# Kernel tuning notes

Measured on AMD Instinct MI355X. Metric: run time of the kernel, lower is better.

The kernel has to match this reference:

```python
import jax, jax.numpy as jnp
import numpy as np

INPUT_DIM = 1024
CODEBOOK_DIM = 128
CODEBOOK_SIZE = 8192
B, N = 8, 4096


def setup_inputs() -> dict:
    key = jax.random.key(0)
    k1, k2, k3 = jax.random.split(key, 3)
    x = jax.random.normal(k1, (B, N, INPUT_DIM), dtype=jnp.float32)
    # xavier_normal_: std = sqrt(2 / (fan_in + fan_out))
    xavier_std = float(np.sqrt(2.0 / (INPUT_DIM + CODEBOOK_DIM)))
    random_projection = jax.random.normal(k2, (INPUT_DIM, CODEBOOK_DIM), dtype=jnp.float32) * xavier_std
    codebook = jax.random.normal(k3, (CODEBOOK_SIZE, CODEBOOK_DIM), dtype=jnp.float32)
    return {"x": x, "random_projection": random_projection, "codebook": codebook}


def reference(x, random_projection, codebook):
    # random projection: [B, N, D] @ [D, E] -> [B, N, E]
    proj = jnp.einsum("bnd,de->bne", x, random_projection)
    b, n, e = proj.shape
    flat = proj.reshape(b * n, e)  # [BN, E]
    eps = 1e-12  # matches torch F.normalize default eps
    nx = flat / jnp.maximum(jnp.linalg.norm(flat, axis=1, keepdims=True), eps)
    ncb = codebook / jnp.maximum(jnp.linalg.norm(codebook, axis=1, keepdims=True), eps)
    # squared euclidean distances [K, BN]; argmin of d^2 == argmin of cdist
    d2 = (
        jnp.sum(ncb * ncb, axis=1)[:, None]
        + jnp.sum(nx * nx, axis=1)[None, :]
        - 2.0 * (ncb @ nx.T)
    )
    nearest = jnp.argmin(d2, axis=0)  # [BN]
    return nearest.reshape(b, n).astype(jnp.int32)
```

## Files before the change

kernel.cpp:

```cpp
#include <hip/hip_runtime.h>
#include <math.h>
#include <float.h>
#include <limits.h>

#define BN      32768
#define D_IN    1024
#define E_DIM   128
#define CB_N    8192

typedef _Float16 f16x8 __attribute__((ext_vector_type(8)));
typedef _Float16 f16x4 __attribute__((ext_vector_type(4)));
typedef float    f32x4 __attribute__((ext_vector_type(4)));


__global__ __launch_bounds__(256) void pack_cb_kernel(
    const float* __restrict__ cb, _Float16* __restrict__ ph,
    _Float16* __restrict__ pl) {
    __shared__ float L[16][129];
    const int t = threadIdx.x;
    const int g = blockIdx.x;

    const int c = t >> 4, p = t & 15;
    const float4 v0 = *(const float4*)&cb[(size_t)(g * 16 + c) * E_DIM + p * 8];
    const float4 v1 = *(const float4*)&cb[(size_t)(g * 16 + c) * E_DIM + p * 8 + 4];
    float ss = v0.x * v0.x + v0.y * v0.y + v0.z * v0.z + v0.w * v0.w
             + v1.x * v1.x + v1.y * v1.y + v1.z * v1.z + v1.w * v1.w;
#pragma unroll
    for (int m = 1; m < 16; m <<= 1) ss += __shfl_xor(ss, m);
    const float inv = 256.0f / fmaxf(sqrtf(ss), 1e-12f);

    L[c][p * 8 + 0] = v0.x * inv; L[c][p * 8 + 1] = v0.y * inv;
    L[c][p * 8 + 2] = v0.z * inv; L[c][p * 8 + 3] = v0.w * inv;
    L[c][p * 8 + 4] = v1.x * inv; L[c][p * 8 + 5] = v1.y * inv;
    L[c][p * 8 + 6] = v1.z * inv; L[c][p * 8 + 7] = v1.w * inv;
    __syncthreads();

    const int kb = t >> 6, lane = t & 63;
    const int quad = (lane >> 4), col = lane & 15;
    f16x8 h, l;
#pragma unroll
    for (int j = 0; j < 8; ++j) {
        const float v = L[col][kb * 32 + quad * 8 + j];
        const _Float16 hv = (_Float16)v;
        h[j] = hv;
        l[j] = (_Float16)(v - (float)hv);
    }
    const size_t off = ((size_t)(g * 4 + kb) * 64 + lane) * 8;
    *(f16x8*)&ph[off] = h;
    *(f16x8*)&pl[off] = l;
}

__global__ __launch_bounds__(64) void pack_rp_kernel(
    const float* __restrict__ rp, _Float16* __restrict__ rph,
    _Float16* __restrict__ rpl) {
    const int b = blockIdx.x;
    const int kb = b >> 3, nt = b & 7;
    const int lane = threadIdx.x;
    const int quad = lane >> 4, col = lane & 15;
    f16x8 h, l;
#pragma unroll
    for (int j = 0; j < 8; ++j) {
        const float v = rp[(size_t)(kb * 32 + quad * 8 + j) * E_DIM + nt * 16 + col] * 64.0f;
        const _Float16 hv = (_Float16)v;
        h[j] = hv;
        l[j] = (_Float16)(v - (float)hv);
    }
    const size_t off = ((size_t)b * 64 + lane) * 8;
    *(f16x8*)&rph[off] = h;
    *(f16x8*)&rpl[off] = l;
}

#define PAD_ROW 40

__global__ __launch_bounds__(256) void proj_kernel(
    const float* __restrict__ x,
    const _Float16* __restrict__ rph, const _Float16* __restrict__ rpl,
    _Float16* __restrict__ qh, _Float16* __restrict__ ql) {
    __shared__ _Float16 Ah[64 * PAD_ROW];
    __shared__ _Float16 Al[64 * PAD_ROW];

    const int tid  = threadIdx.x;
    const int lane = tid & 63;
    const int w    = tid >> 6;
    const int quad = lane >> 4, col = lane & 15;
    const int rbase = blockIdx.x * 64;

    const int srow = tid >> 3;
    const int skc  = (tid & 7) * 4;

    f32x4 acc[4][2];
#pragma unroll
    for (int mt = 0; mt < 4; ++mt)
#pragma unroll
        for (int h = 0; h < 2; ++h) acc[mt][h] = (f32x4){0.f, 0.f, 0.f, 0.f};

    float4 pre[2];
#pragma unroll
    for (int i = 0; i < 2; ++i)
        pre[i] = *(const float4*)&x[(size_t)(rbase + srow + 32 * i) * D_IN + skc];

    for (int kb = 0; kb < 32; ++kb) {
#pragma unroll
        for (int i = 0; i < 2; ++i) {
            const float vv[4] = {pre[i].x, pre[i].y, pre[i].z, pre[i].w};
            f16x4 h4, l4;
#pragma unroll
            for (int j = 0; j < 4; ++j) {
                const float v = vv[j] * 512.0f;
                const _Float16 hv = (_Float16)v;
                h4[j] = hv;
                l4[j] = (_Float16)(v - (float)hv);
            }
            const int base = (srow + 32 * i) * PAD_ROW + skc;
            *(f16x4*)&Ah[base] = h4;
            *(f16x4*)&Al[base] = l4;
        }
        __syncthreads();

        if (kb + 1 < 32) {
#pragma unroll
            for (int i = 0; i < 2; ++i)
                pre[i] = *(const float4*)&x[(size_t)(rbase + srow + 32 * i) * D_IN + (kb + 1) * 32 + skc];
        }

        f16x8 bh[2], bl[2];
#pragma unroll
        for (int h = 0; h < 2; ++h) {
            const int nt = w * 2 + h;
            const size_t off = ((size_t)(kb * 8 + nt) * 64 + lane) * 8;
            bh[h] = *(const f16x8*)&rph[off];
            bl[h] = *(const f16x8*)&rpl[off];
        }

        f16x8 ah[4], al[4];
#pragma unroll
        for (int mt = 0; mt < 4; ++mt) {
            const int base = (mt * 16 + col) * PAD_ROW + quad * 8;
            ah[mt] = *(const f16x8*)&Ah[base];
            al[mt] = *(const f16x8*)&Al[base];
        }

#pragma unroll
        for (int mt = 0; mt < 4; ++mt)
#pragma unroll
            for (int h = 0; h < 2; ++h)
                acc[mt][h] = __builtin_amdgcn_mfma_f32_16x16x32_f16(ah[mt], bh[h], acc[mt][h], 0, 0, 0);
#pragma unroll
        for (int mt = 0; mt < 4; ++mt)
#pragma unroll
            for (int h = 0; h < 2; ++h)
                acc[mt][h] = __builtin_amdgcn_mfma_f32_16x16x32_f16(ah[mt], bl[h], acc[mt][h], 0, 0, 0);
#pragma unroll
        for (int mt = 0; mt < 4; ++mt)
#pragma unroll
            for (int h = 0; h < 2; ++h)
                acc[mt][h] = __builtin_amdgcn_mfma_f32_16x16x32_f16(al[mt], bh[h], acc[mt][h], 0, 0, 0);

        __syncthreads();
    }

#pragma unroll
    for (int mt = 0; mt < 4; ++mt) {
#pragma unroll
        for (int h = 0; h < 2; ++h) {
#pragma unroll
            for (int r = 0; r < 4; ++r) {
                const float v = acc[mt][h][r] * (1.0f / 2048.0f);
                const _Float16 hv = (_Float16)v;
                const _Float16 lv = (_Float16)(v - (float)hv);
                const size_t o = (size_t)(rbase + mt * 16 + quad * 4 + r) * E_DIM
                               + w * 32 + h * 16 + col;
                qh[o] = hv;
                ql[o] = lv;
            }
        }
    }
}

__global__ __launch_bounds__(256, 2) void scores_kernel(
    const _Float16* __restrict__ qh, const _Float16* __restrict__ ql,
    const _Float16* __restrict__ ph, const _Float16* __restrict__ pl,
    int* __restrict__ out) {
    __shared__ float ls[4][64];
    __shared__ int   li[4][64];

    const int tid  = threadIdx.x;
    const int w    = tid >> 6;
    const int lane = tid & 63;
    const int quad = lane >> 4, col = lane & 15;
    const int qb   = blockIdx.x * 64;

    f16x8 ah[4][4], al[4][4];
#pragma unroll
    for (int mt = 0; mt < 4; ++mt)
#pragma unroll
        for (int kb = 0; kb < 4; ++kb) {
            const size_t off = (size_t)(qb + mt * 16 + col) * E_DIM + kb * 32 + quad * 8;
            ah[mt][kb] = *(const f16x8*)&qh[off];
            al[mt][kb] = *(const f16x8*)&ql[off];
        }

    float bs[16];
    int   bi[16];
#pragma unroll
    for (int s = 0; s < 16; ++s) { bs[s] = -FLT_MAX; bi[s] = 0; }

    const int g0 = w * (CB_N / 16 / 4);
    for (int t = 0; t < CB_N / 16 / 4; ++t) {
        const int g = g0 + t;
        f16x8 bh[4], bl[4];
#pragma unroll
        for (int kb = 0; kb < 4; ++kb) {
            const size_t off = ((size_t)(g * 4 + kb) * 64 + lane) * 8;
            bh[kb] = *(const f16x8*)&ph[off];
            bl[kb] = *(const f16x8*)&pl[off];
        }

        f32x4 acc[4];
#pragma unroll
        for (int mt = 0; mt < 4; ++mt) acc[mt] = (f32x4){0.f, 0.f, 0.f, 0.f};

#pragma unroll
        for (int kb = 0; kb < 4; ++kb)
#pragma unroll
            for (int mt = 0; mt < 4; ++mt)
                acc[mt] = __builtin_amdgcn_mfma_f32_16x16x32_f16(ah[mt][kb], bh[kb], acc[mt], 0, 0, 0);
#pragma unroll
        for (int kb = 0; kb < 4; ++kb)
#pragma unroll
            for (int mt = 0; mt < 4; ++mt)
                acc[mt] = __builtin_amdgcn_mfma_f32_16x16x32_f16(ah[mt][kb], bl[kb], acc[mt], 0, 0, 0);
#pragma unroll
        for (int kb = 0; kb < 4; ++kb)
#pragma unroll
            for (int mt = 0; mt < 4; ++mt)
                acc[mt] = __builtin_amdgcn_mfma_f32_16x16x32_f16(al[mt][kb], bh[kb], acc[mt], 0, 0, 0);

        const int code = g * 16 + col;
#pragma unroll
        for (int mt = 0; mt < 4; ++mt)
#pragma unroll
            for (int r = 0; r < 4; ++r) {
                const float v = acc[mt][r];
                const int s = mt * 4 + r;
                if (v > bs[s]) { bs[s] = v; bi[s] = code; }
            }
    }

#pragma unroll
    for (int s = 0; s < 16; ++s) {
#pragma unroll
        for (int m = 1; m < 16; m <<= 1) {
            const float os = __shfl_xor(bs[s], m);
            const int   oi = __shfl_xor(bi[s], m);
            if (os > bs[s] || (os == bs[s] && oi < bi[s])) { bs[s] = os; bi[s] = oi; }
        }
    }

    if (col == 0) {
#pragma unroll
        for (int mt = 0; mt < 4; ++mt)
#pragma unroll
            for (int r = 0; r < 4; ++r) {
                ls[w][mt * 16 + quad * 4 + r] = bs[mt * 4 + r];
                li[w][mt * 16 + quad * 4 + r] = bi[mt * 4 + r];
            }
    }
    __syncthreads();

    if (tid < 64) {
        float s = ls[0][tid];
        int   i = li[0][tid];
#pragma unroll
        for (int ww = 1; ww < 4; ++ww) {
            const float os = ls[ww][tid];
            if (os > s) { s = os; i = li[ww][tid]; }
        }
        out[qb + tid] = i;
    }
}

extern "C" void kernel_launch(void* const* d_in, const int* in_sizes, int n_in,
                              void* d_out, int out_size, void* d_ws, size_t ws_size,
                              hipStream_t stream) {
    const float* x  = (const float*)d_in[0];
    const float* rp = (const float*)d_in[1];
    const float* cb = (const float*)d_in[2];
    int* out = (int*)d_out;

    _Float16* qh  = (_Float16*)d_ws;
    _Float16* ql  = qh  + (size_t)BN * E_DIM;
    _Float16* ph  = ql  + (size_t)BN * E_DIM;
    _Float16* pl  = ph  + (size_t)CB_N * E_DIM;
    _Float16* rph = pl  + (size_t)CB_N * E_DIM;
    _Float16* rpl = rph + (size_t)D_IN * E_DIM;

    pack_cb_kernel<<<CB_N / 16, 256, 0, stream>>>(cb, ph, pl);
    pack_rp_kernel<<<256, 64, 0, stream>>>(rp, rph, rpl);
    proj_kernel<<<BN / 64, 256, 0, stream>>>(x, rph, rpl, qh, ql);
    scores_kernel<<<BN / 64, 256, 0, stream>>>(qh, ql, ph, pl, out);
}
```

Baseline: 419.4 us.

## Fuse projection and codebook scoring into one kernel via shared memory

Merges the projection kernel and the scoring kernel so the projected rows stay in LDS as fp32 and are split into hi/lo fp16 on chip, removing the global write and read of qh/ql. The scoring phase changes its work split: each wave now handles 32 query rows against half the codebook instead of 64 rows against a quarter. It also double-buffers the codebook fragment loads. The trade-off is more LDS per block (about 44KB) with the two-blocks-per-CU bound, and each codebook fragment is now reused by two query tiles per wave instead of four, so codebook traffic per block doubles.

```diff
diff --git a/kernel.cpp b/kernel.cpp
--- a/kernel.cpp
+++ b/kernel.cpp
@@ -71,19 +71,24 @@
 }
 
 #define PAD_ROW 40
-
-__global__ __launch_bounds__(256) void proj_kernel(
+#define PPITCH  132
+
+__global__ __launch_bounds__(256, 2) void fused_kernel(
     const float* __restrict__ x,
     const _Float16* __restrict__ rph, const _Float16* __restrict__ rpl,
-    _Float16* __restrict__ qh, _Float16* __restrict__ ql) {
+    const _Float16* __restrict__ ph, const _Float16* __restrict__ pl,
+    int* __restrict__ out) {
     __shared__ _Float16 Ah[64 * PAD_ROW];
     __shared__ _Float16 Al[64 * PAD_ROW];
+    __shared__ float    P[64 * PPITCH];
+    __shared__ float    ls[4][32];
+    __shared__ int      li[4][32];
 
     const int tid  = threadIdx.x;
     const int lane = tid & 63;
     const int w    = tid >> 6;
     const int quad = lane >> 4, col = lane & 15;
-    const int rbase = blockIdx.x * 64;
+    const int qb   = blockIdx.x * 64;
 
     const int srow = tid >> 3;
     const int skc  = (tid & 7) * 4;
@@ -97,7 +102,7 @@
     float4 pre[2];
 #pragma unroll
     for (int i = 0; i < 2; ++i)
-        pre[i] = *(const float4*)&x[(size_t)(rbase + srow + 32 * i) * D_IN + skc];
+        pre[i] = *(const float4*)&x[(size_t)(qb + srow + 32 * i) * D_IN + skc];
 
     for (int kb = 0; kb < 32; ++kb) {
 #pragma unroll
@@ -120,135 +125,141 @@
         if (kb + 1 < 32) {
 #pragma unroll
             for (int i = 0; i < 2; ++i)
-                pre[i] = *(const float4*)&x[(size_t)(rbase + srow + 32 * i) * D_IN + (kb + 1) * 32 + skc];
-        }
-
-        f16x8 bh[2], bl[2];
+                pre[i] = *(const float4*)&x[(size_t)(qb + srow + 32 * i) * D_IN + (kb + 1) * 32 + skc];
+        }
+
+        f16x8 bh1[2], bl1[2];
 #pragma unroll
         for (int h = 0; h < 2; ++h) {
             const int nt = w * 2 + h;
             const size_t off = ((size_t)(kb * 8 + nt) * 64 + lane) * 8;
-            bh[h] = *(const f16x8*)&rph[off];
-            bl[h] = *(const f16x8*)&rpl[off];
-        }
-
-        f16x8 ah[4], al[4];
+            bh1[h] = *(const f16x8*)&rph[off];
+            bl1[h] = *(const f16x8*)&rpl[off];
+        }
+
+        f16x8 ah1[4], al1[4];
 #pragma unroll
         for (int mt = 0; mt < 4; ++mt) {
             const int base = (mt * 16 + col) * PAD_ROW + quad * 8;
-            ah[mt] = *(const f16x8*)&Ah[base];
-            al[mt] = *(const f16x8*)&Al[base];
+            ah1[mt] = *(const f16x8*)&Ah[base];
+            al1[mt] = *(const f16x8*)&Al[base];
         }
 
 #pragma unroll
         for (int mt = 0; mt < 4; ++mt)
 #pragma unroll
             for (int h = 0; h < 2; ++h)
-                acc[mt][h] = __builtin_amdgcn_mfma_f32_16x16x32_f16(ah[mt], bh[h], acc[mt][h], 0, 0, 0);
+                acc[mt][h] = __builtin_amdgcn_mfma_f32_16x16x32_f16(ah1[mt], bh1[h], acc[mt][h], 0, 0, 0);
 #pragma unroll
         for (int mt = 0; mt < 4; ++mt)
 #pragma unroll
             for (int h = 0; h < 2; ++h)
-                acc[mt][h] = __builtin_amdgcn_mfma_f32_16x16x32_f16(ah[mt], bl[h], acc[mt][h], 0, 0, 0);
+                acc[mt][h] = __builtin_amdgcn_mfma_f32_16x16x32_f16(ah1[mt], bl1[h], acc[mt][h], 0, 0, 0);
 #pragma unroll
         for (int mt = 0; mt < 4; ++mt)
 #pragma unroll
             for (int h = 0; h < 2; ++h)
-                acc[mt][h] = __builtin_amdgcn_mfma_f32_16x16x32_f16(al[mt], bh[h], acc[mt][h], 0, 0, 0);
+                acc[mt][h] = __builtin_amdgcn_mfma_f32_16x16x32_f16(al1[mt], bh1[h], acc[mt][h], 0, 0, 0);
 
         __syncthreads();
     }
 
 #pragma unroll
-    for (int mt = 0; mt < 4; ++mt) {
-#pragma unroll
-        for (int h = 0; h < 2; ++h) {
+    for (int mt = 0; mt < 4; ++mt)
+#pragma unroll
+        for (int h = 0; h < 2; ++h)
 #pragma unroll
             for (int r = 0; r < 4; ++r) {
-                const float v = acc[mt][h][r] * (1.0f / 2048.0f);
-                const _Float16 hv = (_Float16)v;
-                const _Float16 lv = (_Float16)(v - (float)hv);
-                const size_t o = (size_t)(rbase + mt * 16 + quad * 4 + r) * E_DIM
-                               + w * 32 + h * 16 + col;
-                qh[o] = hv;
-                ql[o] = lv;
-            }
-        }
-    }
-}
-
-__global__ __launch_bounds__(256, 2) void scores_kernel(
-    const _Float16* __restrict__ qh, const _Float16* __restrict__ ql,
-    const _Float16* __restrict__ ph, const _Float16* __restrict__ pl,
-    int* __restrict__ out) {
-    __shared__ float ls[4][64];
-    __shared__ int   li[4][64];
-
-    const int tid  = threadIdx.x;
-    const int w    = tid >> 6;
-    const int lane = tid & 63;
-    const int quad = lane >> 4, col = lane & 15;
-    const int qb   = blockIdx.x * 64;
-
-    f16x8 ah[4][4], al[4][4];
-#pragma unroll
-    for (int mt = 0; mt < 4; ++mt)
+                const int row = mt * 16 + quad * 4 + r;
+                const int cc  = w * 32 + h * 16 + col;
+                P[row * PPITCH + cc] = acc[mt][h][r] * (1.0f / 2048.0f);
+            }
+    __syncthreads();
+
+    const int wq = w >> 1;
+    const int wc = w & 1;
+
+    f16x8 ah[2][4], al[2][4];
+#pragma unroll
+    for (int mt2 = 0; mt2 < 2; ++mt2)
 #pragma unroll
         for (int kb = 0; kb < 4; ++kb) {
-            const size_t off = (size_t)(qb + mt * 16 + col) * E_DIM + kb * 32 + quad * 8;
-            ah[mt][kb] = *(const f16x8*)&qh[off];
-            al[mt][kb] = *(const f16x8*)&ql[off];
-        }
-
-    float bs[16];
-    int   bi[16];
-#pragma unroll
-    for (int s = 0; s < 16; ++s) { bs[s] = -FLT_MAX; bi[s] = 0; }
-
-    const int g0 = w * (CB_N / 16 / 4);
-    for (int t = 0; t < CB_N / 16 / 4; ++t) {
-        const int g = g0 + t;
-        f16x8 bh[4], bl[4];
-#pragma unroll
-        for (int kb = 0; kb < 4; ++kb) {
-            const size_t off = ((size_t)(g * 4 + kb) * 64 + lane) * 8;
-            bh[kb] = *(const f16x8*)&ph[off];
-            bl[kb] = *(const f16x8*)&pl[off];
-        }
-
-        f32x4 acc[4];
-#pragma unroll
-        for (int mt = 0; mt < 4; ++mt) acc[mt] = (f32x4){0.f, 0.f, 0.f, 0.f};
+            const int base = (wq * 32 + mt2 * 16 + col) * PPITCH + kb * 32 + quad * 8;
+            const float4 v0 = *(const float4*)&P[base];
+            const float4 v1 = *(const float4*)&P[base + 4];
+            const float vv[8] = {v0.x, v0.y, v0.z, v0.w, v1.x, v1.y, v1.z, v1.w};
+            f16x8 hh, ll;
+#pragma unroll
+            for (int j = 0; j < 8; ++j) {
+                const _Float16 hv = (_Float16)vv[j];
+                hh[j] = hv;
+                ll[j] = (_Float16)(vv[j] - (float)hv);
+            }
+            ah[mt2][kb] = hh;
+            al[mt2][kb] = ll;
+        }
+
+    float bs[8];
+    int   bi[8];
+#pragma unroll
+    for (int s = 0; s < 8; ++s) { bs[s] = -FLT_MAX; bi[s] = 0; }
+
+    const int g0 = wc * 256;
+
+    f16x8 bh[2][4], bl[2][4];
+#pragma unroll
+    for (int kb = 0; kb < 4; ++kb) {
+        const size_t off = ((size_t)(g0 * 4 + kb) * 64 + lane) * 8;
+        bh[0][kb] = *(const f16x8*)&ph[off];
+        bl[0][kb] = *(const f16x8*)&pl[off];
+    }
+
+#pragma unroll 2
+    for (int t = 0; t < 256; ++t) {
+        const int cur = t & 1, nxt = cur ^ 1;
+        if (t + 1 < 256) {
+            const int gn = g0 + t + 1;
+#pragma unroll
+            for (int kb = 0; kb < 4; ++kb) {
+                const size_t off = ((size_t)(gn * 4 + kb) * 64 + lane) * 8;
+                bh[nxt][kb] = *(const f16x8*)&ph[off];
+                bl[nxt][kb] = *(const f16x8*)&pl[off];
+            }
+        }
+
+        f32x4 sacc[2];
+#pragma unroll
+        for (int mt2 = 0; mt2 < 2; ++mt2) sacc[mt2] = (f32x4){0.f, 0.f, 0.f, 0.f};
 
 #pragma unroll
         for (int kb = 0; kb < 4; ++kb)
 #pragma unroll
-            for (int mt = 0; mt < 4; ++mt)
-                acc[mt] = __builtin_amdgcn_mfma_f32_16x16x32_f16(ah[mt][kb], bh[kb], acc[mt], 0, 0, 0);
+            for (int mt2 = 0; mt2 < 2; ++mt2)
+                sacc[mt2] = __builtin_amdgcn_mfma_f32_16x16x32_f16(ah[mt2][kb], bh[cur][kb], sacc[mt2], 0, 0, 0);
 #pragma unroll
         for (int kb = 0; kb < 4; ++kb)
 #pragma unroll
-            for (int mt = 0; mt < 4; ++mt)
-                acc[mt] = __builtin_amdgcn_mfma_f32_16x16x32_f16(ah[mt][kb], bl[kb], acc[mt], 0, 0, 0);
+            for (int mt2 = 0; mt2 < 2; ++mt2)
+                sacc[mt2] = __builtin_amdgcn_mfma_f32_16x16x32_f16(ah[mt2][kb], bl[cur][kb], sacc[mt2], 0, 0, 0);
 #pragma unroll
         for (int kb = 0; kb < 4; ++kb)
 #pragma unroll
-            for (int mt = 0; mt < 4; ++mt)
-                acc[mt] = __builtin_amdgcn_mfma_f32_16x16x32_f16(al[mt][kb], bh[kb], acc[mt], 0, 0, 0);
-
-        const int code = g * 16 + col;
-#pragma unroll
-        for (int mt = 0; mt < 4; ++mt)
+            for (int mt2 = 0; mt2 < 2; ++mt2)
+                sacc[mt2] = __builtin_amdgcn_mfma_f32_16x16x32_f16(al[mt2][kb], bh[cur][kb], sacc[mt2], 0, 0, 0);
+
+        const int code = (g0 + t) * 16 + col;
+#pragma unroll
+        for (int mt2 = 0; mt2 < 2; ++mt2)
 #pragma unroll
             for (int r = 0; r < 4; ++r) {
-                const float v = acc[mt][r];
-                const int s = mt * 4 + r;
+                const float v = sacc[mt2][r];
+                const int s = mt2 * 4 + r;
                 if (v > bs[s]) { bs[s] = v; bi[s] = code; }
             }
     }
 
 #pragma unroll
-    for (int s = 0; s < 16; ++s) {
+    for (int s = 0; s < 8; ++s) {
 #pragma unroll
         for (int m = 1; m < 16; m <<= 1) {
             const float os = __shfl_xor(bs[s], m);
@@ -259,24 +270,24 @@
 
     if (col == 0) {
 #pragma unroll
-        for (int mt = 0; mt < 4; ++mt)
+        for (int mt2 = 0; mt2 < 2; ++mt2)
 #pragma unroll
             for (int r = 0; r < 4; ++r) {
-                ls[w][mt * 16 + quad * 4 + r] = bs[mt * 4 + r];
-                li[w][mt * 16 + quad * 4 + r] = bi[mt * 4 + r];
+                ls[w][mt2 * 16 + quad * 4 + r] = bs[mt2 * 4 + r];
+                li[w][mt2 * 16 + quad * 4 + r] = bi[mt2 * 4 + r];
             }
     }
     __syncthreads();
 
     if (tid < 64) {
-        float s = ls[0][tid];
-        int   i = li[0][tid];
-#pragma unroll
-        for (int ww = 1; ww < 4; ++ww) {
-            const float os = ls[ww][tid];
-            if (os > s) { s = os; i = li[ww][tid]; }
-        }
-        out[qb + tid] = i;
+        const int q   = tid;
+        const int wq2 = q >> 5;
+        const int q32 = q & 31;
+        float s = ls[wq2 * 2 + 0][q32];
+        int   i = li[wq2 * 2 + 0][q32];
+        const float os = ls[wq2 * 2 + 1][q32];
+        if (os > s) { s = os; i = li[wq2 * 2 + 1][q32]; }
+        out[qb + q] = i;
     }
 }
 
@@ -288,15 +299,12 @@
     const float* cb = (const float*)d_in[2];
     int* out = (int*)d_out;
 
-    _Float16* qh  = (_Float16*)d_ws;
-    _Float16* ql  = qh  + (size_t)BN * E_DIM;
-    _Float16* ph  = ql  + (size_t)BN * E_DIM;
+    _Float16* ph  = (_Float16*)d_ws;
     _Float16* pl  = ph  + (size_t)CB_N * E_DIM;
     _Float16* rph = pl  + (size_t)CB_N * E_DIM;
     _Float16* rpl = rph + (size_t)D_IN * E_DIM;
 
     pack_cb_kernel<<<CB_N / 16, 256, 0, stream>>>(cb, ph, pl);
     pack_rp_kernel<<<256, 64, 0, stream>>>(rp, rph, rpl);
-    proj_kernel<<<BN / 64, 256, 0, stream>>>(x, rph, rpl, qh, ql);
-    scores_kernel<<<BN / 64, 256, 0, stream>>>(qh, ql, ph, pl, out);
+    fused_kernel<<<BN / 64, 256, 0, stream>>>(x, rph, rpl, ph, pl, out);
 }
```

Measured after the change: 395.6 us. -5.7%, faster.
